# Kernel tuning notes

Hardware: AMD Instinct MI355X
Metric: run time of the kernel (lower is better)

The kernel has to match this reference:

```python
import jax, jax.numpy as jnp
import numpy as np

N_WAY = 5
K_SHOT = 1
PROJ_DIM = 64
TEMPERATURE = 0.2
EPS_COS = 1e-12   # F.normalize eps in InnerproductSimilarity (cosine)
EPS_L2 = 1e-16    # _l2norm eps


def setup_inputs() -> dict:
    key = jax.random.key(0)
    ks = jax.random.split(key, 8)
    b, q, u, c, h, w = 2, 15, 20, 64, 21, 21
    s = N_WAY * K_SHOT
    std = float(np.sqrt(2.0 / PROJ_DIM))  # kaiming init used for 1x1 conv heads
    return {
        "support_xf": jax.random.normal(ks[0], (b, s, c, h, w), jnp.float32),
        "support_y": jax.random.randint(ks[1], (b, s), 0, N_WAY),
        "query_xf": jax.random.normal(ks[2], (b, q, c, h, w), jnp.float32),
        "query_y": jax.random.randint(ks[3], (b, q), 0, N_WAY),
        "unlabeled_xf": jax.random.normal(ks[4], (b, u, c, h, w), jnp.float32),
        "key_w": jax.random.normal(ks[5], (PROJ_DIM, c), jnp.float32) * std,
        "query_w": jax.random.normal(ks[6], (PROJ_DIM, c), jnp.float32) * std,
        "value_w": jax.random.normal(ks[7], (PROJ_DIM, c), jnp.float32) * std,
    }


def _dual_nn_selection(support_xf, unlabeled_xf):
    """Mutual-NN (dual NN) selection of unlabeled positions per class.
    Returns padded gather indices idx [b,n_way,L], 0/1 validity sel [b,n_way,L], and L.
    L is data-dependent (max per-(batch,class) count), computed eagerly like the
    original torch code's umask_length."""
    b, u, c, h, w = unlabeled_xf.shape
    M_u, M_s = u * h * w, K_SHOT * h * w
    unl = jnp.transpose(unlabeled_xf, (0, 2, 1, 3, 4)).reshape(b, c, M_u)  # [b,c,M_u]
    sup = jnp.transpose(support_xf.reshape(b, N_WAY, K_SHOT, c, h, w), (0, 1, 3, 2, 4, 5)).reshape(b, N_WAY, c, M_s)
    # cosine InnerproductSimilarity: normalize over channel dim
    sup_n = sup / jnp.maximum(jnp.linalg.norm(sup, axis=2, keepdims=True), EPS_COS)
    unl_n = unl / jnp.maximum(jnp.linalg.norm(unl, axis=1, keepdims=True), EPS_COS)
    u2s = jnp.einsum('bcm,bncs->bnms', unl_n, sup_n)  # [b,n_way,M_u,M_s]
    flat = jnp.transpose(u2s, (0, 2, 1, 3)).reshape(b, M_u, N_WAY * M_s)
    s_near = jnp.argmax(flat, axis=1)   # [b, n_way*M_s] nearest unlabeled pos per support slot
    u_near = jnp.argmax(flat, axis=2)   # [b, M_u] nearest support slot per unlabeled pos
    mutual = (jnp.take_along_axis(s_near, u_near, axis=1) == jnp.arange(M_u)[None, :])  # [b,M_u]
    cls = jnp.argmax(jnp.max(u2s, axis=-1), axis=1)  # [b,M_u] class assignment
    umask = jnp.transpose(jax.nn.one_hot(cls, N_WAY, dtype=jnp.float32), (0, 2, 1)) \
            * mutual[:, None, :].astype(jnp.float32)  # [b,n_way,M_u]
    L = int(jnp.max(jnp.sum(umask, axis=-1)))  # umask_length (data-dependent)
    order = jnp.argsort(-umask, axis=-1)       # stable: selected positions first, original order
    idx = order[:, :, :L]                      # [b,n_way,L]
    sel = jnp.take_along_axis(umask, idx, axis=-1)  # 1 = real feature, 0 = zero padding
    return idx, sel, L


def _forward_core(support_xf, query_xf, unlabeled_xf, key_w, query_w, value_w, query_y, idx, sel):
    b, q, c, h, w = query_xf.shape
    hw = h * w
    u = unlabeled_xf.shape[1]
    M_u, M_s = u * hw, K_SHOT * hw
    unl = jnp.transpose(unlabeled_xf, (0, 2, 1, 3, 4)).reshape(b, c, M_u)
    sup = jnp.transpose(support_xf.reshape(b, N_WAY, K_SHOT, c, h, w), (0, 1, 3, 2, 4, 5)).reshape(b, N_WAY, c, M_s)
    # ragged per-class scatter realized as padded gather (zeros where sel==0)
    gathered = jnp.take_along_axis(unl[:, None, :, :], idx[:, :, None, :], axis=-1)  # [b,n_way,c,L]
    unl_dual = gathered * sel[:, :, None, :]
    s_cat_u = jnp.concatenate([sup, unl_dual], axis=-1)  # [b,n_way,c,M_s+L]
    # 1x1 conv heads == channel matmuls
    qf = query_xf.reshape(b, q, c, hw)
    q_proj = jnp.einsum('oc,bqcm->bqom', query_w, qf)   # [b,q,64,hw]
    v_query = jnp.einsum('oc,bqcm->bqom', value_w, qf)  # [b,q,64,hw]
    k_sup = jnp.einsum('oc,bncl->bnol', key_w, s_cat_u)
    v_sup = jnp.einsum('oc,bncl->bnol', value_w, s_cat_u)
    simi = jnp.einsum('bqom,bnol->bqnml', q_proj, k_sup) / np.float32(np.sqrt(PROJ_DIM))  # [b,q,n,hw,Ms+L]
    Lt = simi.shape[-1]
    # _MNN with compensate_for_single == False (encoder == 'FourLayer_64F')
    merged = jnp.transpose(simi, (0, 1, 3, 2, 4)).reshape(b, q, hw, N_WAY * Lt)
    q_near = jnp.argmax(merged, axis=-1)  # [b,q,hw]
    s_near = jnp.argmax(merged, axis=-2)  # [b,q,n_way*Lt]
    q_mask = (jnp.take_along_axis(s_near, q_near, axis=-1) == jnp.arange(hw)[None, None, :]).astype(simi.dtype)
    att = jax.nn.softmax(simi * q_mask[:, :, None, :, None], axis=-1)
    aligned = jnp.einsum('bqnml,bnol->bqnmo', att, v_sup)  # [b,q,n_way,hw,64]
    aligned = aligned / (jnp.linalg.norm(aligned, axis=-1, keepdims=True) + EPS_L2)
    vq = v_query / (jnp.linalg.norm(v_query, axis=2, keepdims=True) + EPS_L2)
    simi2 = (jnp.einsum('bqnmo,bqok->bqnmk', aligned, vq) + 1.0) * 0.5  # FourLayer_64F rescale
    logits = jnp.sum(jnp.max(simi2, axis=-2), axis=-1).reshape(b * q, N_WAY)  # topk(1,-2)+mean == max
    logp = jax.nn.log_softmax(logits / np.float32(TEMPERATURE), axis=-1)
    y = query_y.reshape(b * q)
    return -jnp.mean(jnp.take_along_axis(logp, y[:, None], axis=1))  # CrossEntropyLoss


def reference(support_xf, support_y, query_xf, query_y, unlabeled_xf, key_w, query_w, value_w):
    idx, sel, _ = _dual_nn_selection(support_xf, unlabeled_xf)
    return _forward_core(support_xf, query_xf, unlabeled_xf, key_w, query_w, value_w, query_y, idx, sel)
```

## Files before the change

kernel.cpp:

```cpp
#include <hip/hip_runtime.h>
#include <math.h>

#define B 2
#define Q 15
#define U 20
#define C 64
#define HW 441
#define NW 5
#define MU (U*HW)
#define MS HW
#define NJ (NW*MS)
#define PD 64
#define LCAP NJ
#define LTCAP 896
#define SCAP 896
#define MSP 448
#define NEGF (-3.402823466e38f)

__device__ float g_rnu[B*MU];
__device__ float g_rns[B*NJ];
__device__ unsigned long long g_snearpack[B*NJ];
__device__ unsigned long long g_unearpack[B*MU];
__device__ int   g_counts[B*NW];
__device__ int   g_L[1];
__device__ int   g_selidx[B*NW*LCAP];
__device__ float g_ksup[(size_t)B*NW*PD*LTCAP];
__device__ float g_vsup[(size_t)B*NW*PD*LTCAP];
__device__ float g_vsupT[(size_t)B*NW*LTCAP*PD];
__device__ float g_vbarn[B*NW*PD];
__device__ float g_qproj[(size_t)B*Q*PD*MSP];
__device__ float g_vqn[(size_t)B*Q*PD*MSP];
__device__ unsigned long long g_rowpack[(size_t)B*Q*NW*MSP];
__device__ unsigned long long g_snear2pack[(size_t)B*Q*NW*LTCAP];
__device__ int   g_qmrows[B*Q*MSP];
__device__ int   g_qmcount[B*Q];
__device__ unsigned g_cmax[(size_t)B*Q*NW*MSP];
__device__ float g_logits[B*Q*NW];
__device__ float g_scores[(size_t)B*Q*NW*MSP*SCAP];

__device__ __forceinline__ unsigned enc_f(float f){
  unsigned b=__float_as_uint(f);
  return (b&0x80000000u)? ~b : (b|0x80000000u);
}
__device__ __forceinline__ float dec_f(unsigned k){
  unsigned b=(k&0x80000000u)?(k^0x80000000u):~k;
  return __uint_as_float(b);
}
__device__ __forceinline__ unsigned long long pk_make(float v,int idx){
  return ((unsigned long long)enc_f(v)<<32)|(unsigned)~(unsigned)idx;
}
__device__ __forceinline__ int pk_idx(unsigned long long p){
  return (int)~(unsigned)(p&0xFFFFFFFFull);
}

__global__ void k_init(){
  int i=blockIdx.x*256+threadIdx.x;
  if (i<B*NJ) g_snearpack[i]=0ull;
  if (i<B*MU) g_unearpack[i]=0ull;
  if (i<B*Q*NW*MSP){ g_rowpack[i]=0ull; g_cmax[i]=0u; }
  if (i<B*Q*NW*LTCAP) g_snear2pack[i]=0ull;
  if (i==0) g_L[0]=0;
}

__global__ void k_norms(const float* __restrict__ sup, const float* __restrict__ unl){
  int i=blockIdx.x*256+threadIdx.x;
  if (i<B*MU){
    int b=i/MU, m=i%MU, ui=m/HW, p=m%HW;
    const float* base=unl+((size_t)(b*U+ui)*C)*HW+p;
    float ss=0.f;
    for (int c=0;c<C;c++){ float x=base[(size_t)c*HW]; ss+=x*x; }
    g_rnu[i]=1.f/fmaxf(sqrtf(ss),1e-12f);
  }
  if (i<B*NJ){
    int b=i/NJ, j=i%NJ, n=j/MS, s=j%MS;
    const float* base=sup+((size_t)(b*NW+n)*C)*HW+s;
    float ss=0.f;
    for (int c=0;c<C;c++){ float x=base[(size_t)c*HW]; ss+=x*x; }
    g_rns[i]=1.f/fmaxf(sqrtf(ss),1e-12f);
  }
}

__global__ __launch_bounds__(256) void k_u2s(const float* __restrict__ sup, const float* __restrict__ unl){
  int blk=blockIdx.x;
  int grp=blk%6; blk/=6;
  int rb=blk%138; int b=blk/138;
  int mb=rb*64;
  int tid=threadIdx.x, tm=tid>>4, tl=tid&15;
  int lane=tid&63, w=tid>>6;
  __shared__ __align__(16) float Ut[4096];
  __shared__ __align__(16) float Pt[8192];
  __shared__ unsigned long long colred[512];
  int mv=min(64,MU-mb);
  for (int k=tid;k<4096;k+=256){
    int c=k>>6, mm=k&63; float v=0.f;
    if (mm<mv){ int m=mb+mm, ui=m/HW, p=m%HW; v=unl[((size_t)(b*U+ui)*C+c)*HW+p]*g_rnu[b*MU+m]; }
    Ut[c*64+mm]=v;
  }
  unsigned long long rowpk[4]={0ull,0ull,0ull,0ull};
  for (int t=0;t<3;t++){
    int j0=(grp*3+t)*128;
    int jv=min(128,NJ-j0);
    __syncthreads();
    for (int k=tid;k<8192;k+=256){
      int c=k>>7, jj=k&127; float v=0.f;
      if (jj<jv){ int j=j0+jj, n=j/MS, s=j%MS; v=sup[((size_t)(b*NW+n)*C+c)*HW+s]*g_rns[b*NJ+j]; }
      Pt[c*128+jj]=v;
    }
    __syncthreads();
    float s[4][8]={};
    for (int c=0;c<64;c++){
      float a[4],b0[4],b1[4];
      *(float4*)a =*(const float4*)&Ut[c*64+tm*4];
      *(float4*)b0=*(const float4*)&Pt[c*128+tl*4];
      *(float4*)b1=*(const float4*)&Pt[c*128+64+tl*4];
      #pragma unroll
      for (int i=0;i<4;i++)
        #pragma unroll
        for (int j=0;j<4;j++){ s[i][j]=fmaf(a[i],b0[j],s[i][j]); s[i][j+4]=fmaf(a[i],b1[j],s[i][j+4]); }
    }
    #pragma unroll
    for (int i=0;i<4;i++){
      if (tm*4+i<mv){
        unsigned long long p=rowpk[i];
        #pragma unroll
        for (int j=0;j<8;j++){
          int jj=(j<4)?(tl*4+j):(64+tl*4+(j-4));
          if (jj<jv){
            unsigned long long c2=pk_make(s[i][j],j0+jj);
            if (c2>p) p=c2;
          }
        }
        rowpk[i]=p;
      }
    }
    unsigned long long cpk[8];
    #pragma unroll
    for (int j=0;j<8;j++){
      unsigned long long p=0ull;
      #pragma unroll
      for (int i=0;i<4;i++){
        if (tm*4+i<mv){
          unsigned long long c2=pk_make(s[i][j],mb+tm*4+i);
          if (c2>p) p=c2;
        }
      }
      cpk[j]=p;
    }
    #pragma unroll
    for (int j=0;j<8;j++){
      unsigned long long o;
      o=__shfl_xor(cpk[j],16); if (o>cpk[j]) cpk[j]=o;
      o=__shfl_xor(cpk[j],32); if (o>cpk[j]) cpk[j]=o;
    }
    if ((lane>>4)==0){
      #pragma unroll
      for (int j=0;j<8;j++){
        int jj=(j<4)?(tl*4+j):(64+tl*4+(j-4));
        colred[w*128+jj]=cpk[j];
      }
    }
    __syncthreads();
    if (tid<128 && tid<jv){
      unsigned long long p=colred[tid];
      if (colred[128+tid]>p) p=colred[128+tid];
      if (colred[256+tid]>p) p=colred[256+tid];
      if (colred[384+tid]>p) p=colred[384+tid];
      if (p) atomicMax(&g_snearpack[b*NJ+j0+tid],p);
    }
  }
  #pragma unroll
  for (int i=0;i<4;i++){
    unsigned long long p=rowpk[i];
    #pragma unroll
    for (int mk=1;mk<16;mk<<=1){ unsigned long long o=__shfl_xor(p,mk); if (o>p) p=o; }
    if (tl==0 && tm*4+i<mv && p) atomicMax(&g_unearpack[b*MU+mb+tm*4+i],p);
  }
}

__global__ __launch_bounds__(256) void k_compact(){
  int b=blockIdx.x/NW, n=blockIdx.x%NW;
  int tid=threadIdx.x, lane=tid&63, w=tid>>6;
  __shared__ int wtot[4];
  int base=0;
  for (int m0=0;m0<MU;m0+=256){
    int m=m0+tid;
    bool flag=false;
    if (m<MU){
      int j=pk_idx(g_unearpack[b*MU+m]);
      flag=(j/MS==n) && (pk_idx(g_snearpack[b*NJ+j])==m);
    }
    unsigned long long bal=__ballot(flag);
    if (lane==0) wtot[w]=(int)__popcll(bal);
    __syncthreads();
    int wpre=0, tot=0;
    #pragma unroll
    for (int ww=0;ww<4;ww++){ if (ww<w) wpre+=wtot[ww]; tot+=wtot[ww]; }
    if (flag){
      int pre=(int)__popcll(bal&((1ull<<lane)-1ull));
      g_selidx[(b*NW+n)*LCAP+base+wpre+pre]=m;
    }
    base+=tot;
    __syncthreads();
  }
  if (tid==0){ g_counts[b*NW+n]=base; atomicMax(&g_L[0],base); }
}

__global__ __launch_bounds__(256) void k_kv(const float* __restrict__ sup, const float* __restrict__ unl,
                                            const float* __restrict__ kw, const float* __restrict__ vw){
  int blk=blockIdx.x;
  int lb=blk%(LTCAP/64); blk/=(LTCAP/64);
  int n=blk%NW, b=blk/NW;
  int Lt=MS+g_L[0];
  if (lb*64>=Lt) return;
  int cnt=g_counts[b*NW+n];
  int tid=threadIdx.x, lane=tid&63, w=tid>>6;
  __shared__ float F[4096];
  __shared__ const float* ptr_s[64];
  if (tid<64){
    int l=lb*64+tid;
    const float* p=nullptr;
    if (l<MS) p=&sup[((size_t)(b*NW+n)*C)*HW+l];
    else if (l<MS+cnt){
      int mg=g_selidx[(b*NW+n)*LCAP+(l-MS)];
      int ui=mg/HW, pp=mg%HW;
      p=&unl[((size_t)(b*U+ui)*C)*HW+pp];
    }
    ptr_s[tid]=p;
  }
  __syncthreads();
  for (int k=tid;k<4096;k+=256){
    int c=k>>6, ll=k&63;
    const float* p=ptr_s[ll];
    F[c*64+ll]=p?p[(size_t)c*HW]:0.f;
  }
  __syncthreads();
  int l=lb*64+lane;
  size_t ob=((size_t)(b*NW+n)*PD)*LTCAP+l;
  size_t tb=((size_t)(b*NW+n)*LTCAP+l)*PD;
  for (int oo=0;oo<16;oo++){
    int o=w*16+oo;
    float ka=0.f, va=0.f;
    for (int c=0;c<C;c++){ float f=F[c*64+lane]; ka=fmaf(kw[o*C+c],f,ka); va=fmaf(vw[o*C+c],f,va); }
    g_ksup[ob+(size_t)o*LTCAP]=ka;
    g_vsup[ob+(size_t)o*LTCAP]=va;
    g_vsupT[tb+o]=va;
  }
}

__global__ __launch_bounds__(256) void k_vbar(){
  int bn=blockIdx.x;
  int tid=threadIdx.x, lane=tid&63, w=tid>>6;
  int cnt=g_counts[bn];
  int Lt=MS+g_L[0];
  __shared__ float vb_s[64];
  for (int oo=0;oo<16;oo++){
    int o=w*16+oo;
    const float* row=&g_vsup[((size_t)bn*PD+o)*LTCAP];
    float s=0.f;
    for (int l=lane;l<MS+cnt;l+=64) s+=row[l];
    #pragma unroll
    for (int mk=1;mk<64;mk<<=1) s+=__shfl_xor(s,mk);
    if (lane==0) vb_s[o]=s/(float)Lt;
  }
  __syncthreads();
  if (tid<64){
    float v=vb_s[tid];
    float ss=v*v;
    #pragma unroll
    for (int mk=1;mk<64;mk<<=1) ss+=__shfl_xor(ss,mk);
    g_vbarn[bn*PD+tid]=v/(sqrtf(ss)+1e-16f);
  }
}

__global__ __launch_bounds__(256) void k_qproj(const float* __restrict__ qx, const float* __restrict__ qw,
                                               const float* __restrict__ vw){
  int blk=blockIdx.x;
  int mt=blk%7; blk/=7;
  int bq=blk;
  int tid=threadIdx.x, lane=tid&63, w=tid>>6;
  __shared__ float F[4096];
  __shared__ float ssp[256];
  for (int k=tid;k<4096;k+=256){
    int c=k>>6, mm=k&63, m=mt*64+mm;
    F[c*64+mm]=(m<MS)?qx[((size_t)bq*C+c)*HW+m]:0.f;
  }
  __syncthreads();
  int m=mt*64+lane;
  size_t ob=(size_t)bq*PD*MSP+m;
  float va[16]; float ssl=0.f;
  for (int oo=0;oo<16;oo++){
    int o=w*16+oo;
    float qa=0.f, v=0.f;
    for (int c=0;c<C;c++){ float f=F[c*64+lane]; qa=fmaf(qw[o*C+c],f,qa); v=fmaf(vw[o*C+c],f,v); }
    g_qproj[ob+(size_t)o*MSP]=qa;
    va[oo]=v; ssl=fmaf(v,v,ssl);
  }
  ssp[tid]=ssl;
  __syncthreads();
  float ss=ssp[lane]+ssp[64+lane]+ssp[128+lane]+ssp[192+lane];
  float rn=1.f/(sqrtf(ss)+1e-16f);
  for (int oo=0;oo<16;oo++) g_vqn[ob+(size_t)(w*16+oo)*MSP]=va[oo]*rn;
}

__global__ __launch_bounds__(256) void k_passA(){
  int blk=blockIdx.x;
  int lc=blk%7; blk/=7;
  int mh=blk%4; blk/=4;
  int n=blk%NW; blk/=NW;
  int bq=blk; int b=bq/Q;
  int Lt=MS+g_L[0];
  int nch=(Lt+127)>>7;
  if (lc>=nch) return;
  int l0=lc<<7, lv=min(128,Lt-l0);
  int tid=threadIdx.x, tm=tid>>4, tl=tid&15;
  int lane=tid&63, w=tid>>6;
  int bqn=bq*NW+n;
  int m0=mh*128;
  __shared__ __align__(16) float Qt[32*128];
  __shared__ __align__(16) float Kt[32*128];
  __shared__ unsigned long long colred[512];
  const size_t qb=(size_t)bq*PD*MSP;
  const size_t kb=(size_t)(b*NW+n)*PD*LTCAP;
  float s[8][8]={};
  #pragma unroll
  for (int h=0;h<2;h++){
    __syncthreads();
    for (int k4=tid;k4<1024;k4+=256){
      int o=k4>>5, mq=k4&31;
      int m=m0+mq*4;
      float4 v=make_float4(0.f,0.f,0.f,0.f);
      if (m<MSP) v=*(const float4*)&g_qproj[qb+(size_t)(h*32+o)*MSP+m];
      *(float4*)&Qt[o*128+mq*4]=v;
      *(float4*)&Kt[o*128+mq*4]=*(const float4*)&g_ksup[kb+(size_t)(h*32+o)*LTCAP+l0+mq*4];
    }
    __syncthreads();
    for (int c=0;c<32;c++){
      float a[8],b0[4],b1[4];
      *(float4*)&a[0]=*(const float4*)&Qt[c*128+tm*8];
      *(float4*)&a[4]=*(const float4*)&Qt[c*128+tm*8+4];
      *(float4*)b0=*(const float4*)&Kt[c*128+tl*4];
      *(float4*)b1=*(const float4*)&Kt[c*128+64+tl*4];
      #pragma unroll
      for (int i=0;i<8;i++)
        #pragma unroll
        for (int j=0;j<4;j++){ s[i][j]=fmaf(a[i],b0[j],s[i][j]); s[i][j+4]=fmaf(a[i],b1[j],s[i][j+4]); }
    }
  }
  #pragma unroll
  for (int i=0;i<8;i++)
    #pragma unroll
    for (int j=0;j<8;j++) s[i][j]*=0.125f;
  #pragma unroll
  for (int i=0;i<8;i++){
    int m=m0+tm*8+i;
    if (m<MS){
      size_t sbase=((size_t)bqn*MSP+m)*SCAP+l0;
      *(float4*)&g_scores[sbase+tl*4]   =make_float4(s[i][0],s[i][1],s[i][2],s[i][3]);
      *(float4*)&g_scores[sbase+64+tl*4]=make_float4(s[i][4],s[i][5],s[i][6],s[i][7]);
    }
  }
  #pragma unroll
  for (int i=0;i<8;i++){
    int m=m0+tm*8+i;
    unsigned long long p=0ull;
    if (m<MS){
      #pragma unroll
      for (int j=0;j<8;j++){
        int jj=(j<4)?(tl*4+j):(64+tl*4+(j-4));
        if (jj<lv){
          unsigned long long c2=pk_make(s[i][j],l0+jj);
          if (c2>p) p=c2;
        }
      }
    }
    #pragma unroll
    for (int mk=1;mk<16;mk<<=1){ unsigned long long o=__shfl_xor(p,mk); if (o>p) p=o; }
    if (tl==0 && m<MS && p) atomicMax(&g_rowpack[(size_t)bqn*MSP+m],p);
  }
  #pragma unroll
  for (int j=0;j<8;j++){
    int jj=(j<4)?(tl*4+j):(64+tl*4+(j-4));
    unsigned long long p=0ull;
    #pragma unroll
    for (int i=0;i<8;i++){
      int m=m0+tm*8+i;
      if (m<MS){
        unsigned long long c2=pk_make(s[i][j],m);
        if (c2>p) p=c2;
      }
    }
    {
      unsigned long long o=__shfl_xor(p,16); if (o>p) p=o;
      o=__shfl_xor(p,32); if (o>p) p=o;
    }
    if ((lane>>4)==0) colred[w*128+jj]=p;
  }
  __syncthreads();
  if (tid<128 && tid<lv){
    unsigned long long p=colred[tid];
    if (colred[128+tid]>p) p=colred[128+tid];
    if (colred[256+tid]>p) p=colred[256+tid];
    if (colred[384+tid]>p) p=colred[384+tid];
    if (p) atomicMax(&g_snear2pack[(size_t)bqn*LTCAP+l0+tid],p);
  }
}

__global__ __launch_bounds__(256) void k_qmask(){
  int bq=blockIdx.x;
  int tid=threadIdx.x, lane=tid&63, w=tid>>6;
  __shared__ int wtot[4];
  int base=0;
  for (int m0=0;m0<MS;m0+=256){
    int m=m0+tid;
    bool qm=false;
    if (m<MS){
      unsigned bhv=0u; unsigned long long bp=0ull; int bn=0;
      #pragma unroll
      for (int n=0;n<NW;n++){
        unsigned long long pk=g_rowpack[(size_t)(bq*NW+n)*MSP+m];
        unsigned hv=(unsigned)(pk>>32);
        if (hv>bhv){bhv=hv;bp=pk;bn=n;}
      }
      int bl=pk_idx(bp);
      qm=(pk_idx(g_snear2pack[(size_t)(bq*NW+bn)*LTCAP+bl])==m);
    }
    unsigned long long bal=__ballot(qm);
    if (lane==0) wtot[w]=(int)__popcll(bal);
    __syncthreads();
    int wpre=0, tot=0;
    #pragma unroll
    for (int ww=0;ww<4;ww++){ if (ww<w) wpre+=wtot[ww]; tot+=wtot[ww]; }
    if (qm){
      int pre=(int)__popcll(bal&((1ull<<lane)-1ull));
      g_qmrows[bq*MSP+base+wpre+pre]=m;
    }
    base+=tot;
    __syncthreads();
  }
  if (tid==0) g_qmcount[bq]=base;
}

__global__ __launch_bounds__(256) void k_passB(){
  int blk=blockIdx.x;
  int rt=blk%7; blk/=7;
  int n=blk%NW; blk/=NW;
  int bq=blk; int b=bq/Q;
  int nm=g_qmcount[bq];
  if (rt*64>=nm) return;
  int bqn=bq*NW+n;
  int Lt=MS+g_L[0];
  int nch=(Lt+63)>>6;
  int tid=threadIdx.x, tm=tid>>4, tl=tid&15;
  __shared__ __align__(16) float Vt[4096];
  __shared__ __align__(16) float Pt[64*68];
  __shared__ int rows_s[64];
  if (tid<64){ int g=rt*64+tid; rows_s[tid]=(g<nm)?g_qmrows[bq*MSP+g]:0; }
  __syncthreads();
  float rmax[4]; size_t sb[4];
  #pragma unroll
  for (int i=0;i<4;i++){
    int row=rows_s[tm*4+i];
    rmax[i]=dec_f((unsigned)(g_rowpack[(size_t)bqn*MSP+row]>>32));
    sb[i]=((size_t)bqn*MSP+row)*SCAP;
  }
  const size_t vb=(size_t)(b*NW+n)*LTCAP*PD;
  const size_t qb=(size_t)bq*PD*MSP;
  float lsum[4]={0.f,0.f,0.f,0.f};
  float acc[4][4]={};
  for (int lc=0;lc<nch;lc++){
    int l0=lc<<6, lv=min(64,Lt-l0);
    __syncthreads();
    float4 sv[4];
    #pragma unroll
    for (int i=0;i<4;i++) sv[i]=*(const float4*)&g_scores[sb[i]+l0+tl*4];
    {
      const float* src=&g_vsupT[vb+(size_t)l0*PD];
      #pragma unroll
      for (int it=0;it<4;it++){
        int f4=tid+it*256;
        *(float4*)&Vt[f4*4]=*(const float4*)&src[f4*4];
      }
    }
    #pragma unroll
    for (int i=0;i<4;i++){
      float e0=(tl*4+0<lv)?__expf(sv[i].x-rmax[i]):0.f;
      float e1=(tl*4+1<lv)?__expf(sv[i].y-rmax[i]):0.f;
      float e2=(tl*4+2<lv)?__expf(sv[i].z-rmax[i]):0.f;
      float e3=(tl*4+3<lv)?__expf(sv[i].w-rmax[i]):0.f;
      lsum[i]+=(e0+e1)+(e2+e3);
      *(float4*)&Pt[(tm*4+i)*68+tl*4]=make_float4(e0,e1,e2,e3);
    }
    __syncthreads();
    for (int l4=0;l4<64;l4+=4){
      float4 pq[4];
      #pragma unroll
      for (int i=0;i<4;i++) pq[i]=*(const float4*)&Pt[(tm*4+i)*68+l4];
      #pragma unroll
      for (int u=0;u<4;u++){
        float4 v4=*(const float4*)&Vt[(l4+u)*64+tl*4];
        #pragma unroll
        for (int i=0;i<4;i++){
          float p=((const float*)&pq[i])[u];
          acc[i][0]=fmaf(p,v4.x,acc[i][0]);
          acc[i][1]=fmaf(p,v4.y,acc[i][1]);
          acc[i][2]=fmaf(p,v4.z,acc[i][2]);
          acc[i][3]=fmaf(p,v4.w,acc[i][3]);
        }
      }
    }
  }
  float rn[4];
  #pragma unroll
  for (int i=0;i<4;i++){
    float ls=lsum[i];
    #pragma unroll
    for (int mk=1;mk<16;mk<<=1) ls+=__shfl_xor(ls,mk);
    float ss=0.f;
    #pragma unroll
    for (int j=0;j<4;j++){ acc[i][j]/=ls; ss=fmaf(acc[i][j],acc[i][j],ss); }
    #pragma unroll
    for (int mk=1;mk<16;mk<<=1) ss+=__shfl_xor(ss,mk);
    rn[i]=1.f/(sqrtf(ss)+1e-16f);
  }
  __syncthreads();
  #pragma unroll
  for (int i=0;i<4;i++)
    *(float4*)&Pt[(tm*4+i)*68+tl*4]=make_float4(acc[i][0],acc[i][1],acc[i][2],acc[i][3]);
  int rowok[4];
  #pragma unroll
  for (int i=0;i<4;i++) rowok[i]=(rt*64+tm*4+i<nm);
  for (int kt=0;kt<7;kt++){
    __syncthreads();
    for (int k=tid;k<1024;k+=256){
      int o=k>>4, kq=k&15;
      *(float4*)&Vt[o*64+kq*4]=*(const float4*)&g_vqn[qb+(size_t)o*MSP+kt*64+kq*4];
    }
    __syncthreads();
    float d[4][4]={};
    for (int o=0;o<64;o++){
      float a[4], bv4[4];
      #pragma unroll
      for (int i=0;i<4;i++) a[i]=Pt[(tm*4+i)*68+o];
      *(float4*)bv4=*(const float4*)&Vt[o*64+tl*4];
      #pragma unroll
      for (int i=0;i<4;i++)
        #pragma unroll
        for (int j=0;j<4;j++) d[i][j]=fmaf(a[i],bv4[j],d[i][j]);
    }
    #pragma unroll
    for (int j=0;j<4;j++){
      int kg=kt*64+tl*4+j;
      float mv=NEGF;
      #pragma unroll
      for (int i=0;i<4;i++) if (rowok[i]) mv=fmaxf(mv,d[i][j]*rn[i]);
      mv=fmaxf(mv,__shfl_xor(mv,16));
      mv=fmaxf(mv,__shfl_xor(mv,32));
      if (((tid>>4)&3)==0 && kg<MS && mv>-1e37f)
        atomicMax(&g_cmax[(size_t)bqn*MSP+kg],enc_f(mv));
    }
  }
}

__global__ __launch_bounds__(256) void k_logits(){
  int bqn=blockIdx.x;
  int n=bqn%NW, bq=bqn/NW, b=bq/Q;
  int tid=threadIdx.x;
  int nm=g_qmcount[bq];
  __shared__ float red[256];
  __shared__ float vb_s[64];
  if (tid<64) vb_s[tid]=g_vbarn[(b*NW+n)*PD+tid];
  __syncthreads();
  const float* vq=&g_vqn[(size_t)bq*PD*MSP];
  float p=0.f;
  for (int k=tid;k<MS;k+=256){
    float v=dec_f(g_cmax[(size_t)bqn*MSP+k]);
    if (nm<MS){
      float d=0.f;
      for (int o=0;o<PD;o++) d=fmaf(vb_s[o],vq[(size_t)o*MSP+k],d);
      v=fmaxf(v,d);
    }
    p+=(v+1.f)*0.5f;
  }
  red[tid]=p; __syncthreads();
  for (int s=128;s;s>>=1){ if (tid<s) red[tid]+=red[tid+s]; __syncthreads(); }
  if (tid==0) g_logits[bqn]=red[0];
}

__global__ void k_loss(const int* __restrict__ qy, float* __restrict__ out){
  int t=threadIdx.x;
  float lp=0.f;
  if (t<B*Q){
    int y=qy[t];
    float xv[NW]; float mxv=NEGF;
    #pragma unroll
    for (int n=0;n<NW;n++){ xv[n]=g_logits[t*NW+n]*5.f; mxv=fmaxf(mxv,xv[n]); }
    float s=0.f, xy=0.f;
    #pragma unroll
    for (int n=0;n<NW;n++){ s+=__expf(xv[n]-mxv); if (n==y) xy=xv[n]; }
    lp=xy-mxv-logf(s);
  }
  #pragma unroll
  for (int off=32;off;off>>=1) lp+=__shfl_down(lp,off);
  if (t==0) out[0]=-lp/(float)(B*Q);
}

extern "C" void kernel_launch(void* const* d_in, const int* in_sizes, int n_in,
                              void* d_out, int out_size, void* d_ws, size_t ws_size,
                              hipStream_t stream) {
  (void)in_sizes; (void)n_in; (void)out_size; (void)d_ws; (void)ws_size;
  const float* sup=(const float*)d_in[0];
  const float* qx =(const float*)d_in[2];
  const int*   qy =(const int*)d_in[3];
  const float* unl=(const float*)d_in[4];
  const float* kw =(const float*)d_in[5];
  const float* qw =(const float*)d_in[6];
  const float* vw =(const float*)d_in[7];
  float* out=(float*)d_out;

  k_init   <<<525,256,0,stream>>>();
  k_norms  <<<69,256,0,stream>>>(sup,unl);
  k_u2s    <<<B*138*6,256,0,stream>>>(sup,unl);
  k_compact<<<B*NW,256,0,stream>>>();
  k_kv     <<<B*NW*(LTCAP/64),256,0,stream>>>(sup,unl,kw,vw);
  k_vbar   <<<B*NW,256,0,stream>>>();
  k_qproj  <<<B*Q*7,256,0,stream>>>(qx,qw,vw);
  k_passA  <<<B*Q*NW*28,256,0,stream>>>();
  k_qmask  <<<B*Q,256,0,stream>>>();
  k_passB  <<<B*Q*NW*7,256,0,stream>>>();
  k_logits <<<B*Q*NW,256,0,stream>>>();
  k_loss   <<<1,64,0,stream>>>(qy,out);
}
```

Before: 717.6 us.

## Pre-normalize inputs into padded layouts and retile u2s similarity as 128x128 blocks

k_norms now writes normalized unlabeled and support features into padded, channel-major buffers, zeroing the padding in k_init. k_u2s then loads them with float4 copies instead of gathering with div/mod indexing and per-element scaling. The similarity kernel is retiled from 64-row blocks looping over three 128-column chunks to 128x128 output tiles with an 8x8 per-thread register block, split over two 32-channel stages. The aim is to cut redundant global gathers and raise arithmetic intensity. In exchange it adds an extra global write and read of the normalized data, higher register pressure, and more atomics per block.

```diff
diff --git a/kernel.cpp b/kernel.cpp
--- a/kernel.cpp
+++ b/kernel.cpp
@@ -15,15 +15,17 @@
 #define LTCAP 896
 #define SCAP 896
 #define MSP 448
+#define MUP 8832
+#define NJP 2304
 #define NEGF (-3.402823466e38f)
 
-__device__ float g_rnu[B*MU];
-__device__ float g_rns[B*NJ];
 __device__ unsigned long long g_snearpack[B*NJ];
 __device__ unsigned long long g_unearpack[B*MU];
 __device__ int   g_counts[B*NW];
 __device__ int   g_L[1];
 __device__ int   g_selidx[B*NW*LCAP];
+__device__ float g_unln[(size_t)B*C*MUP];
+__device__ float g_supn[(size_t)B*C*NJP];
 __device__ float g_ksup[(size_t)B*NW*PD*LTCAP];
 __device__ float g_vsup[(size_t)B*NW*PD*LTCAP];
 __device__ float g_vsupT[(size_t)B*NW*LTCAP*PD];
@@ -59,6 +61,14 @@
   if (i<B*MU) g_unearpack[i]=0ull;
   if (i<B*Q*NW*MSP){ g_rowpack[i]=0ull; g_cmax[i]=0u; }
   if (i<B*Q*NW*LTCAP) g_snear2pack[i]=0ull;
+  if (i<B*C*(MUP-MU)){
+    int b=i/(C*(MUP-MU)), r=i%(C*(MUP-MU)), c=r/(MUP-MU), m=MU+r%(MUP-MU);
+    g_unln[((size_t)b*C+c)*MUP+m]=0.f;
+  }
+  if (i<B*C*(NJP-NJ)){
+    int b=i/(C*(NJP-NJ)), r=i%(C*(NJP-NJ)), c=r/(NJP-NJ), j=NJ+r%(NJP-NJ);
+    g_supn[((size_t)b*C+c)*NJP+j]=0.f;
+  }
   if (i==0) g_L[0]=0;
 }
 
@@ -69,111 +79,98 @@
     const float* base=unl+((size_t)(b*U+ui)*C)*HW+p;
     float ss=0.f;
     for (int c=0;c<C;c++){ float x=base[(size_t)c*HW]; ss+=x*x; }
-    g_rnu[i]=1.f/fmaxf(sqrtf(ss),1e-12f);
+    float rn=1.f/fmaxf(sqrtf(ss),1e-12f);
+    for (int c=0;c<C;c++) g_unln[((size_t)b*C+c)*MUP+m]=base[(size_t)c*HW]*rn;
   }
   if (i<B*NJ){
     int b=i/NJ, j=i%NJ, n=j/MS, s=j%MS;
     const float* base=sup+((size_t)(b*NW+n)*C)*HW+s;
     float ss=0.f;
     for (int c=0;c<C;c++){ float x=base[(size_t)c*HW]; ss+=x*x; }
-    g_rns[i]=1.f/fmaxf(sqrtf(ss),1e-12f);
-  }
-}
-
-__global__ __launch_bounds__(256) void k_u2s(const float* __restrict__ sup, const float* __restrict__ unl){
+    float rn=1.f/fmaxf(sqrtf(ss),1e-12f);
+    for (int c=0;c<C;c++) g_supn[((size_t)b*C+c)*NJP+j]=base[(size_t)c*HW]*rn;
+  }
+}
+
+__global__ __launch_bounds__(256) void k_u2s(){
   int blk=blockIdx.x;
-  int grp=blk%6; blk/=6;
-  int rb=blk%138; int b=blk/138;
-  int mb=rb*64;
+  int jc=blk%18; blk/=18;
+  int rb=blk%69; int b=blk/69;
+  int m0=rb*128, j0=jc*128;
+  int mv=min(128,MU-m0);
+  int jv=min(128,NJ-j0);
   int tid=threadIdx.x, tm=tid>>4, tl=tid&15;
   int lane=tid&63, w=tid>>6;
-  __shared__ __align__(16) float Ut[4096];
-  __shared__ __align__(16) float Pt[8192];
+  __shared__ __align__(16) float Ut[32*128];
+  __shared__ __align__(16) float Pt[32*128];
   __shared__ unsigned long long colred[512];
-  int mv=min(64,MU-mb);
-  for (int k=tid;k<4096;k+=256){
-    int c=k>>6, mm=k&63; float v=0.f;
-    if (mm<mv){ int m=mb+mm, ui=m/HW, p=m%HW; v=unl[((size_t)(b*U+ui)*C+c)*HW+p]*g_rnu[b*MU+m]; }
-    Ut[c*64+mm]=v;
-  }
-  unsigned long long rowpk[4]={0ull,0ull,0ull,0ull};
-  for (int t=0;t<3;t++){
-    int j0=(grp*3+t)*128;
-    int jv=min(128,NJ-j0);
-    __syncthreads();
-    for (int k=tid;k<8192;k+=256){
-      int c=k>>7, jj=k&127; float v=0.f;
-      if (jj<jv){ int j=j0+jj, n=j/MS, s=j%MS; v=sup[((size_t)(b*NW+n)*C+c)*HW+s]*g_rns[b*NJ+j]; }
-      Pt[c*128+jj]=v;
-    }
-    __syncthreads();
-    float s[4][8]={};
-    for (int c=0;c<64;c++){
-      float a[4],b0[4],b1[4];
-      *(float4*)a =*(const float4*)&Ut[c*64+tm*4];
+  const size_t ub=(size_t)b*C*MUP+m0;
+  const size_t pb=(size_t)b*C*NJP+j0;
+  float s[8][8]={};
+  #pragma unroll
+  for (int h=0;h<2;h++){
+    __syncthreads();
+    for (int k4=tid;k4<1024;k4+=256){
+      int c=k4>>5, mq=k4&31;
+      *(float4*)&Ut[c*128+mq*4]=*(const float4*)&g_unln[ub+(size_t)(h*32+c)*MUP+mq*4];
+      *(float4*)&Pt[c*128+mq*4]=*(const float4*)&g_supn[pb+(size_t)(h*32+c)*NJP+mq*4];
+    }
+    __syncthreads();
+    for (int c=0;c<32;c++){
+      float a[8],b0[4],b1[4];
+      *(float4*)&a[0]=*(const float4*)&Ut[c*128+tm*8];
+      *(float4*)&a[4]=*(const float4*)&Ut[c*128+tm*8+4];
       *(float4*)b0=*(const float4*)&Pt[c*128+tl*4];
       *(float4*)b1=*(const float4*)&Pt[c*128+64+tl*4];
       #pragma unroll
-      for (int i=0;i<4;i++)
+      for (int i=0;i<8;i++)
         #pragma unroll
         for (int j=0;j<4;j++){ s[i][j]=fmaf(a[i],b0[j],s[i][j]); s[i][j+4]=fmaf(a[i],b1[j],s[i][j+4]); }
     }
-    #pragma unroll
-    for (int i=0;i<4;i++){
-      if (tm*4+i<mv){
-        unsigned long long p=rowpk[i];
-        #pragma unroll
-        for (int j=0;j<8;j++){
-          int jj=(j<4)?(tl*4+j):(64+tl*4+(j-4));
-          if (jj<jv){
-            unsigned long long c2=pk_make(s[i][j],j0+jj);
-            if (c2>p) p=c2;
-          }
-        }
-        rowpk[i]=p;
-      }
-    }
-    unsigned long long cpk[8];
-    #pragma unroll
-    for (int j=0;j<8;j++){
-      unsigned long long p=0ull;
-      #pragma unroll
-      for (int i=0;i<4;i++){
-        if (tm*4+i<mv){
-          unsigned long long c2=pk_make(s[i][j],mb+tm*4+i);
+  }
+  #pragma unroll
+  for (int i=0;i<8;i++){
+    int mm=tm*8+i;
+    unsigned long long p=0ull;
+    if (mm<mv){
+      #pragma unroll
+      for (int j=0;j<8;j++){
+        int jj=(j<4)?(tl*4+j):(64+tl*4+(j-4));
+        if (jj<jv){
+          unsigned long long c2=pk_make(s[i][j],j0+jj);
           if (c2>p) p=c2;
         }
       }
-      cpk[j]=p;
-    }
-    #pragma unroll
-    for (int j=0;j<8;j++){
-      unsigned long long o;
-      o=__shfl_xor(cpk[j],16); if (o>cpk[j]) cpk[j]=o;
-      o=__shfl_xor(cpk[j],32); if (o>cpk[j]) cpk[j]=o;
-    }
-    if ((lane>>4)==0){
-      #pragma unroll
-      for (int j=0;j<8;j++){
-        int jj=(j<4)?(tl*4+j):(64+tl*4+(j-4));
-        colred[w*128+jj]=cpk[j];
+    }
+    #pragma unroll
+    for (int mk=1;mk<16;mk<<=1){ unsigned long long o=__shfl_xor(p,mk); if (o>p) p=o; }
+    if (tl==0 && mm<mv && p) atomicMax(&g_unearpack[b*MU+m0+mm],p);
+  }
+  #pragma unroll
+  for (int j=0;j<8;j++){
+    int jj=(j<4)?(tl*4+j):(64+tl*4+(j-4));
+    unsigned long long p=0ull;
+    #pragma unroll
+    for (int i=0;i<8;i++){
+      int mm=tm*8+i;
+      if (mm<mv){
+        unsigned long long c2=pk_make(s[i][j],m0+mm);
+        if (c2>p) p=c2;
       }
     }
-    __syncthreads();
-    if (tid<128 && tid<jv){
-      unsigned long long p=colred[tid];
-      if (colred[128+tid]>p) p=colred[128+tid];
-      if (colred[256+tid]>p) p=colred[256+tid];
-      if (colred[384+tid]>p) p=colred[384+tid];
-      if (p) atomicMax(&g_snearpack[b*NJ+j0+tid],p);
-    }
-  }
-  #pragma unroll
-  for (int i=0;i<4;i++){
-    unsigned long long p=rowpk[i];
-    #pragma unroll
-    for (int mk=1;mk<16;mk<<=1){ unsigned long long o=__shfl_xor(p,mk); if (o>p) p=o; }
-    if (tl==0 && tm*4+i<mv && p) atomicMax(&g_unearpack[b*MU+mb+tm*4+i],p);
+    {
+      unsigned long long o=__shfl_xor(p,16); if (o>p) p=o;
+      o=__shfl_xor(p,32); if (o>p) p=o;
+    }
+    if ((lane>>4)==0) colred[w*128+jj]=p;
+  }
+  __syncthreads();
+  if (tid<128 && tid<jv){
+    unsigned long long p=colred[tid];
+    if (colred[128+tid]>p) p=colred[128+tid];
+    if (colred[256+tid]>p) p=colred[256+tid];
+    if (colred[384+tid]>p) p=colred[384+tid];
+    if (p) atomicMax(&g_snearpack[b*NJ+j0+tid],p);
   }
 }
 
@@ -619,7 +616,7 @@
 
   k_init   <<<525,256,0,stream>>>();
   k_norms  <<<69,256,0,stream>>>(sup,unl);
-  k_u2s    <<<B*138*6,256,0,stream>>>(sup,unl);
+  k_u2s    <<<B*69*18,256,0,stream>>>();
   k_compact<<<B*NW,256,0,stream>>>();
   k_kv     <<<B*NW*(LTCAP/64),256,0,stream>>>(sup,unl,kw,vw);
   k_vbar   <<<B*NW,256,0,stream>>>();
```

After: 659.4 us. 1.09x faster.
